# Kernel optimization log

Hardware: AMD Instinct MI355X
Metric: run time of the kernel (lower is better)

The kernel has to match this reference:

```python
import jax, jax.numpy as jnp
import numpy as np
import math

IN_DIM = 2048
OUT_DIM = 2048
BATCH = 4096
BN_EPS = 1e-5


def setup_inputs() -> dict:
    key = jax.random.key(0)
    ks = jax.random.split(key, 6)
    x = jax.random.normal(ks[0], (BATCH, IN_DIM), dtype=jnp.float32)
    # scale ~ N(1.0, 0.1), translate = 0
    scale = 1.0 + 0.1 * jax.random.normal(ks[1], (1, IN_DIM), dtype=jnp.float32)
    translate = jnp.zeros((1, IN_DIM), dtype=jnp.float32)
    # kaiming-normal-ish init for wave_weight (fan_in), orthogonal-ish for base_weight
    wave_weight = jax.random.normal(ks[2], (OUT_DIM, IN_DIM), dtype=jnp.float32) * np.sqrt(2.0 / IN_DIM)
    bw = jax.random.normal(ks[3], (OUT_DIM, IN_DIM), dtype=jnp.float32)
    q, _ = jnp.linalg.qr(bw.T)  # (IN_DIM, OUT_DIM) orthonormal columns
    base_weight = q.T.astype(jnp.float32)
    gamma = jnp.ones((OUT_DIM,), dtype=jnp.float32)
    beta = jnp.zeros((OUT_DIM,), dtype=jnp.float32)
    return {"x": x, "scale": scale, "translate": translate,
            "wave_weight": wave_weight, "base_weight": base_weight,
            "gamma": gamma, "beta": beta}


def reference(x, scale, translate, wave_weight, base_weight, gamma, beta):
    # Bio wavelet: pi^-1/4 * cos(3u) * exp(-0.5 u^2), u = (x - t) / clamp(s, 1e-3)
    u = (x - translate) / jnp.maximum(scale, 1e-3)            # (B, in)
    wavelet = (math.pi ** -0.25) * jnp.cos(3.0 * u) * jnp.exp(-0.5 * u * u)
    # einsum 'boi,oi->bo' with singleton o broadcast == plain matmul
    wave_out = jnp.einsum('bi,oi->bo', wavelet, wave_weight)  # (B, out)
    base_out = jnp.einsum('bi,oi->bo', x, base_weight)        # (B, out)
    y = wave_out + 0.3 * base_out
    # BatchNorm1d (training mode: batch statistics, biased variance)
    mean = jnp.mean(y, axis=0)
    var = jnp.mean(jnp.square(y - mean), axis=0)
    out = gamma * (y - mean) * jax.lax.rsqrt(var + BN_EPS) + beta
    # dropout treated as identity (deterministic reference)
    return out
```

## Files before the change

kernel.cpp:

```cpp
#include <hip/hip_runtime.h>
#include <stdint.h>

#define IN_DIM 2048
#define OUT_DIM 2048
#define BATCH 4096
#define KDIM (2 * IN_DIM)
#define KROWB (KDIM * 2)
#define BN_EPS 1e-5f

typedef __attribute__((ext_vector_type(8))) short bf16x8;
typedef __attribute__((ext_vector_type(4))) float f32x4;

__device__ __forceinline__ unsigned short f2bf(float f) {
  union { float f; unsigned u; } v; v.f = f;
  unsigned r = v.u + 0x7FFFu + ((v.u >> 16) & 1u);
  return (unsigned short)(r >> 16);
}

__global__ void prep_act(const float* __restrict__ x,
                         const float* __restrict__ scale,
                         const float* __restrict__ translate,
                         unsigned short* __restrict__ A) {
  int e = (blockIdx.x * 256 + threadIdx.x) * 4;
  int b = e / IN_DIM;
  int i = e % IN_DIM;
  float4 xv = *(const float4*)(x + e);
  float4 sv = *(const float4*)(scale + i);
  float4 tv = *(const float4*)(translate + i);
  const float c = 0.7511255444649425f;
  float u0 = (xv.x - tv.x) / fmaxf(sv.x, 1e-3f);
  float u1 = (xv.y - tv.y) / fmaxf(sv.y, 1e-3f);
  float u2 = (xv.z - tv.z) / fmaxf(sv.z, 1e-3f);
  float u3 = (xv.w - tv.w) / fmaxf(sv.w, 1e-3f);
  ushort4 wv, xb;
  wv.x = f2bf(c * __cosf(3.0f * u0) * __expf(-0.5f * u0 * u0));
  wv.y = f2bf(c * __cosf(3.0f * u1) * __expf(-0.5f * u1 * u1));
  wv.z = f2bf(c * __cosf(3.0f * u2) * __expf(-0.5f * u2 * u2));
  wv.w = f2bf(c * __cosf(3.0f * u3) * __expf(-0.5f * u3 * u3));
  xb.x = f2bf(xv.x); xb.y = f2bf(xv.y); xb.z = f2bf(xv.z); xb.w = f2bf(xv.w);
  *(ushort4*)(A + (size_t)b * KDIM + i) = wv;
  *(ushort4*)(A + (size_t)b * KDIM + IN_DIM + i) = xb;
}

__global__ void prep_w(const float* __restrict__ ww,
                       const float* __restrict__ bw,
                       unsigned short* __restrict__ W) {
  int e = (blockIdx.x * 256 + threadIdx.x) * 4;
  int o = e / IN_DIM;
  int k = e % IN_DIM;
  float4 a = *(const float4*)(ww + e);
  float4 b = *(const float4*)(bw + e);
  ushort4 wa, wb;
  wa.x = f2bf(a.x); wa.y = f2bf(a.y); wa.z = f2bf(a.z); wa.w = f2bf(a.w);
  wb.x = f2bf(0.3f * b.x); wb.y = f2bf(0.3f * b.y);
  wb.z = f2bf(0.3f * b.z); wb.w = f2bf(0.3f * b.w);
  *(ushort4*)(W + (size_t)o * KDIM + k) = wa;
  *(ushort4*)(W + (size_t)o * KDIM + IN_DIM + k) = wb;
}


#define GLDS(gp, lo) __builtin_amdgcn_global_load_lds( \
    (const __attribute__((address_space(1))) void*)(gp), \
    (__attribute__((address_space(3))) void*)(lds + (lo) + ldsw), 16, 0, 0)

#define MM16(mh) do { \
  __builtin_amdgcn_s_setprio(1); \
  _Pragma("unroll") for (int i2 = 0; i2 < 4; ++i2) \
  _Pragma("unroll") for (int j2 = 0; j2 < 4; ++j2) \
    acc[(mh) * 4 + i2][j2] = __builtin_amdgcn_mfma_f32_16x16x32_bf16( \
        af[i2], bq[j2], acc[(mh) * 4 + i2][j2], 0, 0, 0); \
  __builtin_amdgcn_s_setprio(0); \
} while (0)

#define LGKM0() asm volatile("s_waitcnt lgkmcnt(0)" ::: "memory")
#define VMW6()  asm volatile("s_waitcnt vmcnt(6)" ::: "memory")
#define VMW0()  asm volatile("s_waitcnt vmcnt(0)" ::: "memory")
#define NOW()   do { } while (0)
#define BAR()   do { asm volatile("" ::: "memory"); __builtin_amdgcn_s_barrier(); \
                     asm volatile("" ::: "memory"); } while (0)

#define KT(S, SS, TOFS, DOST, TAILW) do { \
  const char* Lr = lds + gbase + (S) * 24576; \
  af[0] = *(const bf16x8*)(Lr + aoff + 0 * 1024 + roff); \
  af[1] = *(const bf16x8*)(Lr + aoff + 1 * 1024 + roff); \
  af[2] = *(const bf16x8*)(Lr + aoff + 2 * 1024 + roff); \
  af[3] = *(const bf16x8*)(Lr + aoff + 3 * 1024 + roff); \
  bq[0] = *(const bf16x8*)(Lr + boff + 0 * 1024 + roff); \
  bq[1] = *(const bf16x8*)(Lr + boff + 1 * 1024 + roff); \
  bq[2] = *(const bf16x8*)(Lr + boff + 2 * 1024 + roff); \
  bq[3] = *(const bf16x8*)(Lr + boff + 3 * 1024 + roff); \
  if (DOST) { \
    GLDS(aG + (TOFS),               gbase + (SS) * 24576 + 0); \
    GLDS(aG + (TOFS) +  64 * KROWB, gbase + (SS) * 24576 + 4096); \
    GLDS(aG + (TOFS) + 128 * KROWB, gbase + (SS) * 24576 + 8192); \
    GLDS(aG + (TOFS) + 192 * KROWB, gbase + (SS) * 24576 + 12288); \
    GLDS(bG + (TOFS),               gbase + (SS) * 24576 + 16384); \
    GLDS(bG + (TOFS) +  64 * KROWB, gbase + (SS) * 24576 + 20480); \
  } \
  MM16(0); \
  af[0] = *(const bf16x8*)(Lr + aoff + 4096 + 0 * 1024 + roff); \
  af[1] = *(const bf16x8*)(Lr + aoff + 4096 + 1 * 1024 + roff); \
  af[2] = *(const bf16x8*)(Lr + aoff + 4096 + 2 * 1024 + roff); \
  af[3] = *(const bf16x8*)(Lr + aoff + 4096 + 3 * 1024 + roff); \
  MM16(1); \
  LGKM0(); TAILW; BAR(); \
} while (0)

__global__ __launch_bounds__(512, 2) void gemm_ksplit(
    const unsigned short* __restrict__ A,
    const unsigned short* __restrict__ W,
    float* __restrict__ Y,
    float* __restrict__ sums, float* __restrict__ sqs) {
  __shared__ char lds[147456];
  const int tid = threadIdx.x;
  const int lane = tid & 63;
  const int g = tid >> 8;
  const int gt = tid & 255;
  const int w4 = (tid >> 6) & 3;
  const int wm = w4 >> 1;
  const int wn = w4 & 1;
  const int gbase = g * 73728;

  const int xcd = blockIdx.x & 7;
  const int li = blockIdx.x >> 3;
  const int brow = ((xcd >> 1) * 4 + (li >> 3)) * 256;
  const int bcol = ((xcd & 1) * 8 + (li & 7)) * 128;

  const int srow2 = 2 * (gt >> 3) + ((gt >> 2) & 1);
  const int sksl = (gt & 3) ^ ((gt >> 3) & 3);
  const char* aG = (const char*)A + (size_t)(brow + srow2) * KROWB + g * 4096 + sksl * 16;
  const char* bG = (const char*)W + (size_t)(bcol + srow2) * KROWB + g * 4096 + sksl * 16;
  const int ldsw = w4 * 1024;

  const int lh = (lane & 15) >> 1;
  const int roff = lh * 128 + (lane & 1) * 64 + (((lane >> 4) ^ (lh & 3)) << 4);
  const int aoff = wm * 8192;
  const int boff = 16384 + wn * 4096;

  f32x4 acc[8][4];
#pragma unroll
  for (int m = 0; m < 8; ++m)
#pragma unroll
    for (int n = 0; n < 4; ++n)
      acc[m][n] = (f32x4){0.f, 0.f, 0.f, 0.f};
  bf16x8 af[4], bq[4];

  GLDS(aG, gbase + 0); GLDS(aG + 64 * KROWB, gbase + 4096);
  GLDS(aG + 128 * KROWB, gbase + 8192); GLDS(aG + 192 * KROWB, gbase + 12288);
  GLDS(bG, gbase + 16384); GLDS(bG + 64 * KROWB, gbase + 20480);
  GLDS(aG + 64, gbase + 24576);
  GLDS(aG + 64 * KROWB + 64, gbase + 24576 + 4096);
  GLDS(aG + 128 * KROWB + 64, gbase + 24576 + 8192);
  GLDS(aG + 192 * KROWB + 64, gbase + 24576 + 12288);
  GLDS(bG + 64, gbase + 24576 + 16384);
  GLDS(bG + 64 * KROWB + 64, gbase + 24576 + 20480);
  VMW6(); BAR();

  for (int tt = 0; tt < 60; tt += 3) {
    KT(0, 2, (tt + 2) * 64, 1, VMW6());
    KT(1, 0, (tt + 3) * 64, 1, VMW6());
    KT(2, 1, (tt + 4) * 64, 1, VMW6());
  }
  KT(0, 2, 62 * 64, 1, VMW6());
  KT(1, 0, 63 * 64, 1, VMW6());
  KT(2, 0, 0, 0, VMW0());
  KT(0, 0, 0, 0, NOW());

  if (g == 1) {
#pragma unroll
    for (int m = 0; m < 8; ++m)
#pragma unroll
      for (int n = 0; n < 4; ++n)
        *(f32x4*)(lds + w4 * 32768 + (m * 4 + n) * 1024 + lane * 16) = acc[m][n];
  }
  LGKM0(); BAR();
  if (g == 0) {
#pragma unroll
    for (int m = 0; m < 8; ++m)
#pragma unroll
      for (int n = 0; n < 4; ++n) {
        f32x4 p = *(const f32x4*)(lds + w4 * 32768 + (m * 4 + n) * 1024 + lane * 16);
        acc[m][n] += p;
      }

    const int r0 = brow + wm * 128 + (lane >> 4) * 4;
    const int c0 = bcol + wn * 64 + (lane & 15);
#pragma unroll
    for (int m = 0; m < 8; ++m)
#pragma unroll
      for (int n = 0; n < 4; ++n)
#pragma unroll
        for (int j = 0; j < 4; ++j)
          Y[(size_t)(r0 + m * 16 + j) * OUT_DIM + (c0 + n * 16)] = acc[m][n][j];

#pragma unroll
    for (int n = 0; n < 4; ++n) {
      float s = 0.f, q = 0.f;
#pragma unroll
      for (int m = 0; m < 8; ++m)
#pragma unroll
        for (int j = 0; j < 4; ++j) {
          float v = acc[m][n][j];
          s += v; q += v * v;
        }
      s += __shfl_xor(s, 16); q += __shfl_xor(q, 16);
      s += __shfl_xor(s, 32); q += __shfl_xor(q, 32);
      if (lane < 16) {
        atomicAdd(&sums[c0 + n * 16], s);
        atomicAdd(&sqs[c0 + n * 16], q);
      }
    }
  }
}

__global__ void bnorm(float* __restrict__ Y,
                      const float* __restrict__ sums, const float* __restrict__ sqs,
                      const float* __restrict__ gamma, const float* __restrict__ beta) {
  int e = (blockIdx.x * 256 + threadIdx.x) * 4;
  int c = e % OUT_DIM;
  float4 y = *(float4*)(Y + e);
  float4 s = *(const float4*)(sums + c);
  float4 q = *(const float4*)(sqs + c);
  float4 g = *(const float4*)(gamma + c);
  float4 bb = *(const float4*)(beta + c);
  const float invB = 1.0f / (float)BATCH;
  float m0 = s.x * invB, m1 = s.y * invB, m2 = s.z * invB, m3 = s.w * invB;
  float i0 = rsqrtf(q.x * invB - m0 * m0 + BN_EPS);
  float i1 = rsqrtf(q.y * invB - m1 * m1 + BN_EPS);
  float i2 = rsqrtf(q.z * invB - m2 * m2 + BN_EPS);
  float i3 = rsqrtf(q.w * invB - m3 * m3 + BN_EPS);
  y.x = g.x * (y.x - m0) * i0 + bb.x;
  y.y = g.y * (y.y - m1) * i1 + bb.y;
  y.z = g.z * (y.z - m2) * i2 + bb.z;
  y.w = g.w * (y.w - m3) * i3 + bb.w;
  *(float4*)(Y + e) = y;
}

extern "C" void kernel_launch(void* const* d_in, const int* in_sizes, int n_in,
                              void* d_out, int out_size, void* d_ws, size_t ws_size,
                              hipStream_t stream) {
  const float* x         = (const float*)d_in[0];
  const float* scale     = (const float*)d_in[1];
  const float* translate = (const float*)d_in[2];
  const float* ww        = (const float*)d_in[3];
  const float* bw        = (const float*)d_in[4];
  const float* gamma     = (const float*)d_in[5];
  const float* beta      = (const float*)d_in[6];
  float* out = (float*)d_out;

  char* ws = (char*)d_ws;
  unsigned short* A = (unsigned short*)ws;
  unsigned short* W = (unsigned short*)(ws + 33554432);
  float* sums = (float*)(ws + 50331648);
  float* sqs  = sums + OUT_DIM;

  hipMemsetAsync(sums, 0, 2 * OUT_DIM * sizeof(float), stream);
  prep_act<<<(BATCH * IN_DIM) / 1024, 256, 0, stream>>>(x, scale, translate, A);
  prep_w<<<(OUT_DIM * IN_DIM) / 1024, 256, 0, stream>>>(ww, bw, W);
  gemm_ksplit<<<256, 512, 0, stream>>>(A, W, out, sums, sqs);
  bnorm<<<(BATCH * OUT_DIM) / 1024, 256, 0, stream>>>(out, sums, sqs, gamma, beta);
}
```

Baseline: 110.1 us.

## Replace in-block K-split 256x128 GEMM with 128x128 tiles of two waves

The GEMM kernel drops the in-block K-split, where two groups of 4 waves each reduced half of K on a 256x128 tile and combined partials through LDS. It becomes a 128x128-tile kernel with 2 waves per block, 512 blocks, and each wave owning a 64x128 sub-tile across the full K. This removes the LDS partial-sum reduction and cuts shared memory per block, allowing more blocks per CU. In exchange, each wave has far fewer waves to hide latency, the tile is smaller so global traffic per FLOP rises, and the loop runs twice as many K iterations.

```diff
diff --git a/kernel.cpp b/kernel.cpp
--- a/kernel.cpp
+++ b/kernel.cpp
@@ -63,152 +63,129 @@
     (const __attribute__((address_space(1))) void*)(gp), \
     (__attribute__((address_space(3))) void*)(lds + (lo) + ldsw), 16, 0, 0)
 
-#define MM16(mh) do { \
+#define MM32() do { \
   __builtin_amdgcn_s_setprio(1); \
   _Pragma("unroll") for (int i2 = 0; i2 < 4; ++i2) \
-  _Pragma("unroll") for (int j2 = 0; j2 < 4; ++j2) \
-    acc[(mh) * 4 + i2][j2] = __builtin_amdgcn_mfma_f32_16x16x32_bf16( \
-        af[i2], bq[j2], acc[(mh) * 4 + i2][j2], 0, 0, 0); \
+  _Pragma("unroll") for (int j2 = 0; j2 < 8; ++j2) \
+    acc[i2][j2] = __builtin_amdgcn_mfma_f32_16x16x32_bf16( \
+        af[i2], bq[j2], acc[i2][j2], 0, 0, 0); \
   __builtin_amdgcn_s_setprio(0); \
 } while (0)
 
 #define LGKM0() asm volatile("s_waitcnt lgkmcnt(0)" ::: "memory")
-#define VMW6()  asm volatile("s_waitcnt vmcnt(6)" ::: "memory")
+#define VMW8()  asm volatile("s_waitcnt vmcnt(8)" ::: "memory")
 #define VMW0()  asm volatile("s_waitcnt vmcnt(0)" ::: "memory")
 #define NOW()   do { } while (0)
 #define BAR()   do { asm volatile("" ::: "memory"); __builtin_amdgcn_s_barrier(); \
                      asm volatile("" ::: "memory"); } while (0)
 
 #define KT(S, SS, TOFS, DOST, TAILW) do { \
-  const char* Lr = lds + gbase + (S) * 24576; \
+  const char* Lr = lds + (S) * 16384; \
   af[0] = *(const bf16x8*)(Lr + aoff + 0 * 1024 + roff); \
   af[1] = *(const bf16x8*)(Lr + aoff + 1 * 1024 + roff); \
   af[2] = *(const bf16x8*)(Lr + aoff + 2 * 1024 + roff); \
   af[3] = *(const bf16x8*)(Lr + aoff + 3 * 1024 + roff); \
-  bq[0] = *(const bf16x8*)(Lr + boff + 0 * 1024 + roff); \
-  bq[1] = *(const bf16x8*)(Lr + boff + 1 * 1024 + roff); \
-  bq[2] = *(const bf16x8*)(Lr + boff + 2 * 1024 + roff); \
-  bq[3] = *(const bf16x8*)(Lr + boff + 3 * 1024 + roff); \
+  bq[0] = *(const bf16x8*)(Lr + 8192 + 0 * 1024 + roff); \
+  bq[1] = *(const bf16x8*)(Lr + 8192 + 1 * 1024 + roff); \
+  bq[2] = *(const bf16x8*)(Lr + 8192 + 2 * 1024 + roff); \
+  bq[3] = *(const bf16x8*)(Lr + 8192 + 3 * 1024 + roff); \
+  bq[4] = *(const bf16x8*)(Lr + 8192 + 4 * 1024 + roff); \
+  bq[5] = *(const bf16x8*)(Lr + 8192 + 5 * 1024 + roff); \
+  bq[6] = *(const bf16x8*)(Lr + 8192 + 6 * 1024 + roff); \
+  bq[7] = *(const bf16x8*)(Lr + 8192 + 7 * 1024 + roff); \
   if (DOST) { \
-    GLDS(aG + (TOFS),               gbase + (SS) * 24576 + 0); \
-    GLDS(aG + (TOFS) +  64 * KROWB, gbase + (SS) * 24576 + 4096); \
-    GLDS(aG + (TOFS) + 128 * KROWB, gbase + (SS) * 24576 + 8192); \
-    GLDS(aG + (TOFS) + 192 * KROWB, gbase + (SS) * 24576 + 12288); \
-    GLDS(bG + (TOFS),               gbase + (SS) * 24576 + 16384); \
-    GLDS(bG + (TOFS) +  64 * KROWB, gbase + (SS) * 24576 + 20480); \
+    GLDS(aG + (TOFS),              (SS) * 16384 + 0); \
+    GLDS(aG + (TOFS) + 32 * KROWB, (SS) * 16384 + 2048); \
+    GLDS(aG + (TOFS) + 64 * KROWB, (SS) * 16384 + 4096); \
+    GLDS(aG + (TOFS) + 96 * KROWB, (SS) * 16384 + 6144); \
+    GLDS(bG + (TOFS),              (SS) * 16384 + 8192); \
+    GLDS(bG + (TOFS) + 32 * KROWB, (SS) * 16384 + 10240); \
+    GLDS(bG + (TOFS) + 64 * KROWB, (SS) * 16384 + 12288); \
+    GLDS(bG + (TOFS) + 96 * KROWB, (SS) * 16384 + 14336); \
   } \
-  MM16(0); \
-  af[0] = *(const bf16x8*)(Lr + aoff + 4096 + 0 * 1024 + roff); \
-  af[1] = *(const bf16x8*)(Lr + aoff + 4096 + 1 * 1024 + roff); \
-  af[2] = *(const bf16x8*)(Lr + aoff + 4096 + 2 * 1024 + roff); \
-  af[3] = *(const bf16x8*)(Lr + aoff + 4096 + 3 * 1024 + roff); \
-  MM16(1); \
+  MM32(); \
   LGKM0(); TAILW; BAR(); \
 } while (0)
 
-__global__ __launch_bounds__(512, 2) void gemm_ksplit(
+__global__ __launch_bounds__(128, 1) void gemm128(
     const unsigned short* __restrict__ A,
     const unsigned short* __restrict__ W,
     float* __restrict__ Y,
     float* __restrict__ sums, float* __restrict__ sqs) {
-  __shared__ char lds[147456];
+  __shared__ char lds[49152];
   const int tid = threadIdx.x;
   const int lane = tid & 63;
-  const int g = tid >> 8;
-  const int gt = tid & 255;
-  const int w4 = (tid >> 6) & 3;
-  const int wm = w4 >> 1;
-  const int wn = w4 & 1;
-  const int gbase = g * 73728;
+  const int w = tid >> 6;
 
   const int xcd = blockIdx.x & 7;
   const int li = blockIdx.x >> 3;
-  const int brow = ((xcd >> 1) * 4 + (li >> 3)) * 256;
-  const int bcol = ((xcd & 1) * 8 + (li & 7)) * 128;
-
-  const int srow2 = 2 * (gt >> 3) + ((gt >> 2) & 1);
-  const int sksl = (gt & 3) ^ ((gt >> 3) & 3);
-  const char* aG = (const char*)A + (size_t)(brow + srow2) * KROWB + g * 4096 + sksl * 16;
-  const char* bG = (const char*)W + (size_t)(bcol + srow2) * KROWB + g * 4096 + sksl * 16;
-  const int ldsw = w4 * 1024;
+  const int bcol = (xcd * 2 + (li >> 5)) * 128;
+  const int brow = (li & 31) * 128;
+
+  const int srow2 = 2 * (tid >> 3) + ((tid >> 2) & 1);
+  const int sksl = (tid & 3) ^ ((tid >> 3) & 3);
+  const char* aG = (const char*)A + (size_t)(brow + srow2) * KROWB + sksl * 16;
+  const char* bG = (const char*)W + (size_t)(bcol + srow2) * KROWB + sksl * 16;
+  const int ldsw = w * 1024;
 
   const int lh = (lane & 15) >> 1;
   const int roff = lh * 128 + (lane & 1) * 64 + (((lane >> 4) ^ (lh & 3)) << 4);
-  const int aoff = wm * 8192;
-  const int boff = 16384 + wn * 4096;
-
-  f32x4 acc[8][4];
-#pragma unroll
-  for (int m = 0; m < 8; ++m)
-#pragma unroll
-    for (int n = 0; n < 4; ++n)
+  const int aoff = w * 4096;
+
+  f32x4 acc[4][8];
+#pragma unroll
+  for (int m = 0; m < 4; ++m)
+#pragma unroll
+    for (int n = 0; n < 8; ++n)
       acc[m][n] = (f32x4){0.f, 0.f, 0.f, 0.f};
-  bf16x8 af[4], bq[4];
-
-  GLDS(aG, gbase + 0); GLDS(aG + 64 * KROWB, gbase + 4096);
-  GLDS(aG + 128 * KROWB, gbase + 8192); GLDS(aG + 192 * KROWB, gbase + 12288);
-  GLDS(bG, gbase + 16384); GLDS(bG + 64 * KROWB, gbase + 20480);
-  GLDS(aG + 64, gbase + 24576);
-  GLDS(aG + 64 * KROWB + 64, gbase + 24576 + 4096);
-  GLDS(aG + 128 * KROWB + 64, gbase + 24576 + 8192);
-  GLDS(aG + 192 * KROWB + 64, gbase + 24576 + 12288);
-  GLDS(bG + 64, gbase + 24576 + 16384);
-  GLDS(bG + 64 * KROWB + 64, gbase + 24576 + 20480);
-  VMW6(); BAR();
-
-  for (int tt = 0; tt < 60; tt += 3) {
-    KT(0, 2, (tt + 2) * 64, 1, VMW6());
-    KT(1, 0, (tt + 3) * 64, 1, VMW6());
-    KT(2, 1, (tt + 4) * 64, 1, VMW6());
+  bf16x8 af[4], bq[8];
+
+  GLDS(aG, 0); GLDS(aG + 32 * KROWB, 2048);
+  GLDS(aG + 64 * KROWB, 4096); GLDS(aG + 96 * KROWB, 6144);
+  GLDS(bG, 8192); GLDS(bG + 32 * KROWB, 10240);
+  GLDS(bG + 64 * KROWB, 12288); GLDS(bG + 96 * KROWB, 14336);
+  GLDS(aG + 64, 16384); GLDS(aG + 32 * KROWB + 64, 16384 + 2048);
+  GLDS(aG + 64 * KROWB + 64, 16384 + 4096); GLDS(aG + 96 * KROWB + 64, 16384 + 6144);
+  GLDS(bG + 64, 16384 + 8192); GLDS(bG + 32 * KROWB + 64, 16384 + 10240);
+  GLDS(bG + 64 * KROWB + 64, 16384 + 12288); GLDS(bG + 96 * KROWB + 64, 16384 + 14336);
+  VMW8(); BAR();
+
+  for (int tt = 0; tt < 123; tt += 3) {
+    KT(0, 2, (tt + 2) * 64, 1, VMW8());
+    KT(1, 0, (tt + 3) * 64, 1, VMW8());
+    KT(2, 1, (tt + 4) * 64, 1, VMW8());
   }
-  KT(0, 2, 62 * 64, 1, VMW6());
-  KT(1, 0, 63 * 64, 1, VMW6());
-  KT(2, 0, 0, 0, VMW0());
-  KT(0, 0, 0, 0, NOW());
-
-  if (g == 1) {
-#pragma unroll
-    for (int m = 0; m < 8; ++m)
-#pragma unroll
-      for (int n = 0; n < 4; ++n)
-        *(f32x4*)(lds + w4 * 32768 + (m * 4 + n) * 1024 + lane * 16) = acc[m][n];
-  }
-  LGKM0(); BAR();
-  if (g == 0) {
-#pragma unroll
-    for (int m = 0; m < 8; ++m)
-#pragma unroll
-      for (int n = 0; n < 4; ++n) {
-        f32x4 p = *(const f32x4*)(lds + w4 * 32768 + (m * 4 + n) * 1024 + lane * 16);
-        acc[m][n] += p;
+  KT(0, 2, 125 * 64, 1, VMW8());
+  KT(1, 0, 126 * 64, 1, VMW8());
+  KT(2, 1, 127 * 64, 1, VMW8());
+  KT(0, 0, 0, 0, VMW0());
+  KT(1, 0, 0, 0, NOW());
+
+  const int r0 = brow + w * 64 + (lane >> 4) * 4;
+  const int c0 = bcol + (lane & 15);
+#pragma unroll
+  for (int m = 0; m < 4; ++m)
+#pragma unroll
+    for (int n = 0; n < 8; ++n)
+#pragma unroll
+      for (int j = 0; j < 4; ++j)
+        Y[(size_t)(r0 + m * 16 + j) * OUT_DIM + (c0 + n * 16)] = acc[m][n][j];
+
+#pragma unroll
+  for (int n = 0; n < 8; ++n) {
+    float s = 0.f, q = 0.f;
+#pragma unroll
+    for (int m = 0; m < 4; ++m)
+#pragma unroll
+      for (int j = 0; j < 4; ++j) {
+        float v = acc[m][n][j];
+        s += v; q += v * v;
       }
-
-    const int r0 = brow + wm * 128 + (lane >> 4) * 4;
-    const int c0 = bcol + wn * 64 + (lane & 15);
-#pragma unroll
-    for (int m = 0; m < 8; ++m)
-#pragma unroll
-      for (int n = 0; n < 4; ++n)
-#pragma unroll
-        for (int j = 0; j < 4; ++j)
-          Y[(size_t)(r0 + m * 16 + j) * OUT_DIM + (c0 + n * 16)] = acc[m][n][j];
-
-#pragma unroll
-    for (int n = 0; n < 4; ++n) {
-      float s = 0.f, q = 0.f;
-#pragma unroll
-      for (int m = 0; m < 8; ++m)
-#pragma unroll
-        for (int j = 0; j < 4; ++j) {
-          float v = acc[m][n][j];
-          s += v; q += v * v;
-        }
-      s += __shfl_xor(s, 16); q += __shfl_xor(q, 16);
-      s += __shfl_xor(s, 32); q += __shfl_xor(q, 32);
-      if (lane < 16) {
-        atomicAdd(&sums[c0 + n * 16], s);
-        atomicAdd(&sqs[c0 + n * 16], q);
-      }
+    s += __shfl_xor(s, 16); q += __shfl_xor(q, 16);
+    s += __shfl_xor(s, 32); q += __shfl_xor(q, 32);
+    if (lane < 16) {
+      atomicAdd(&sums[c0 + n * 16], s);
+      atomicAdd(&sqs[c0 + n * 16], q);
     }
   }
 }
@@ -257,6 +234,6 @@
   hipMemsetAsync(sums, 0, 2 * OUT_DIM * sizeof(float), stream);
   prep_act<<<(BATCH * IN_DIM) / 1024, 256, 0, stream>>>(x, scale, translate, A);
   prep_w<<<(OUT_DIM * IN_DIM) / 1024, 256, 0, stream>>>(ww, bw, W);
-  gemm_ksplit<<<256, 512, 0, stream>>>(A, W, out, sums, sqs);
+  gemm128<<<512, 128, 0, stream>>>(A, W, out, sums, sqs);
   bnorm<<<(BATCH * OUT_DIM) / 1024, 256, 0, stream>>>(out, sums, sqs, gamma, beta);
 }
```

Result: slower. 120.2 us (+9.2%).
